# Kernel optimization log

Hardware: AMD Instinct MI355X
Metric: run time of the kernel (lower is better)

The kernel has to match this reference:

```python
import jax, jax.numpy as jnp
import numpy as np

N_NODES = 50000
N_EDGES = 800000
D_IN = 64
N_CLASSES = 2


def _glorot(key, shape):
    lim = float(np.sqrt(6.0 / (shape[0] + shape[1])))
    return jax.random.uniform(key, shape, jnp.float32, -lim, lim)


def setup_inputs() -> dict:
    key = jax.random.key(0)
    ks = jax.random.split(key, 12)
    x = jax.random.normal(ks[0], (N_NODES, D_IN), jnp.float32)
    edge_index = jax.random.randint(ks[1], (2, N_EDGES), 0, N_NODES, jnp.int64)
    return {
        "x": x,
        "edge_index": edge_index,
        # SAGEConv1: 64 -> 16 (lin_l on aggregated neighbors, lin_r on root)
        "w1_n": _glorot(ks[2], (D_IN, 16)), "w1_r": _glorot(ks[3], (D_IN, 16)), "b1": jnp.zeros((16,), jnp.float32),
        # SAGEConv2: 16 -> 32
        "w2_n": _glorot(ks[4], (16, 32)), "w2_r": _glorot(ks[5], (16, 32)), "b2": jnp.zeros((32,), jnp.float32),
        # MLP head
        "fw1": _glorot(ks[6], (32, 64)), "fb1": jnp.zeros((64,), jnp.float32),
        "fw2": _glorot(ks[7], (64, 128)), "fb2": jnp.zeros((128,), jnp.float32),
        "fw3": _glorot(ks[8], (128, N_CLASSES)), "fb3": jnp.zeros((N_CLASSES,), jnp.float32),
    }


def _sage_conv(x, src, dst, w_n, w_r, b):
    # mean aggregation of source-node features onto destination nodes
    msg_sum = jax.ops.segment_sum(x[src], dst, num_segments=N_NODES)  # [N, d]
    deg = jax.ops.segment_sum(jnp.ones((src.shape[0],), x.dtype), dst, num_segments=N_NODES)
    agg = msg_sum / jnp.clip(deg, 1.0)[:, None]
    return agg @ w_n + x @ w_r + b


def reference(x, edge_index, w1_n, w1_r, b1, w2_n, w2_r, b2, fw1, fb1, fw2, fb2, fw3, fb3):
    src, dst = edge_index[0], edge_index[1]
    h = jax.nn.relu(_sage_conv(x, src, dst, w1_n, w1_r, b1))
    h = jax.nn.relu(_sage_conv(h, src, dst, w2_n, w2_r, b2))
    h = jax.nn.relu(h @ fw1 + fb1)
    h = jax.nn.relu(h @ fw2 + fb2)  # dropout omitted (eval mode)
    return h @ fw3 + fb3
```

## Files before the change

kernel.cpp:

```cpp
#include <hip/hip_runtime.h>
#include <hip/hip_fp16.h>

#define N_NODES 50000
#define N_EDGES 800000
#define MAXD 64
#define BSHIFT 7
#define BNODES 128
#define NBUCKET 391
#define NSCB 128
#define EPB (N_EDGES / NSCB)
#define RCAP 64
#define LIN1B ((N_NODES + 63) / 64)

typedef _Float16 f16x8 __attribute__((ext_vector_type(8)));
typedef float f32x4 __attribute__((ext_vector_type(4)));

union H8 { uint4 v; unsigned int u[4]; f16x8 h; };

__device__ __forceinline__ f32x4 MM(const H8& a, const H8& b, f32x4 c) {
    return __builtin_amdgcn_mfma_f32_16x16x32_f16(a.h, b.h, c, 0, 0, 0);
}
__device__ __forceinline__ unsigned int pkh(float a, float b) {
    __half2 h = __floats2half2_rn(a, b);
    unsigned int u;
    __builtin_memcpy(&u, &h, 4);
    return u;
}

__global__ __launch_bounds__(256) void k_scat_lin1(
        const int* __restrict__ src, const int* __restrict__ dst,
        unsigned int* __restrict__ staging, int* __restrict__ counts,
        const float* __restrict__ x,
        const float* __restrict__ w1n, const float* __restrict__ w1r,
        const float* __restrict__ b1,
        __half* __restrict__ xw1n, __half* __restrict__ xr1b) {
    __shared__ __align__(16) unsigned char smem[4608];
    const int tid = threadIdx.x;

    if (blockIdx.x < NSCB) {
        int* lh = (int*)smem;
        for (int i = tid; i < NBUCKET; i += 256) lh[i] = 0;
        __syncthreads();
        const int sb = blockIdx.x;
        const int base = sb * EPB;
        for (int i = tid; i < EPB; i += 256) {
            int d = dst[base + i], s = src[base + i];
            int b = d >> BSHIFT;
            int pos = atomicAdd(&lh[b], 1);
            if (pos < RCAP)
                staging[(b * NSCB + sb) * RCAP + pos] =
                    ((unsigned int)(d & (BNODES - 1)) << 16) | (unsigned int)s;
        }
        __syncthreads();
        for (int i = tid; i < NBUCKET; i += 256)
            counts[i * NSCB + sb] = min(lh[i], RCAP);
    } else {
        __half* s_w1t = (__half*)smem;
        for (int i = tid; i < 2048; i += 256) {
            int o = i & 31, k = i >> 5;
            float v = (o < 16) ? w1n[k * 16 + o] : w1r[k * 16 + (o - 16)];
            s_w1t[o * 72 + k] = __float2half(v);
        }
        __syncthreads();
        const int l = tid & 63, li = l & 15, g = l >> 4;
        const int wid = tid >> 6;
        const int node = (blockIdx.x - NSCB) * 64 + wid * 16 + li;
        const int nodec = node < N_NODES ? node : N_NODES - 1;

        H8 B0, B1;
        {
            const float4* xp = (const float4*)(x + nodec * 64 + 8 * g);
            float4 v0 = xp[0], v1 = xp[1];
            B0.u[0] = pkh(v0.x, v0.y); B0.u[1] = pkh(v0.z, v0.w);
            B0.u[2] = pkh(v1.x, v1.y); B0.u[3] = pkh(v1.z, v1.w);
            const float4* xq = (const float4*)(x + nodec * 64 + 32 + 8 * g);
            float4 w0 = xq[0], w1 = xq[1];
            B1.u[0] = pkh(w0.x, w0.y); B1.u[1] = pkh(w0.z, w0.w);
            B1.u[2] = pkh(w1.x, w1.y); B1.u[3] = pkh(w1.z, w1.w);
        }
        H8 A;
        f32x4 c0 = {0.f, 0.f, 0.f, 0.f};
        A.v = *(const uint4*)(s_w1t + li * 72 + 8 * g);
        c0 = MM(A, B0, c0);
        A.v = *(const uint4*)(s_w1t + li * 72 + 32 + 8 * g);
        c0 = MM(A, B1, c0);
        f32x4 c1 = *(const f32x4*)(b1 + 4 * g);
        A.v = *(const uint4*)(s_w1t + (16 + li) * 72 + 8 * g);
        c1 = MM(A, B0, c1);
        A.v = *(const uint4*)(s_w1t + (16 + li) * 72 + 32 + 8 * g);
        c1 = MM(A, B1, c1);

        if (node < N_NODES) {
            uint2 s0, s1;
            s0.x = pkh(c0[0], c0[1]); s0.y = pkh(c0[2], c0[3]);
            s1.x = pkh(c1[0], c1[1]); s1.y = pkh(c1[2], c1[3]);
            *(uint2*)(xw1n + node * 16 + 4 * g) = s0;
            *(uint2*)(xr1b + node * 16 + 4 * g) = s1;
        }
    }
}

__global__ __launch_bounds__(256) void k_build(
        const unsigned int* __restrict__ staging, const int* __restrict__ counts,
        unsigned int* __restrict__ nbrU, int* __restrict__ deg) {
    __shared__ unsigned short ltbl[BNODES * MAXD];
    __shared__ int lcnt[BNODES];
    __shared__ int lc[NSCB];
    const int tid = threadIdx.x, b = blockIdx.x;
    if (tid < BNODES) lcnt[tid] = 0;
    for (int i = tid; i < NSCB; i += 256) lc[i] = counts[b * NSCB + i];
    __syncthreads();
    for (int i = tid; i < NSCB * RCAP; i += 256) {
        int sb = i >> 6, j = i & 63;
        if (j < lc[sb]) {
            unsigned int u = staging[(b * NSCB + sb) * RCAP + j];
            int dl = u >> 16, s = u & 0xFFFF;
            int slot = atomicAdd(&lcnt[dl], 1);
            if (slot < MAXD) ltbl[(dl << 6) + slot] = (unsigned short)s;
        }
    }
    __syncthreads();
    const int nbase = b << BSHIFT;
    for (int i = tid; i < BNODES * 32; i += 256) {
        int nl = i >> 5, j = i & 31;
        int node = nbase + nl;
        if (node < N_NODES && 2 * j < lcnt[nl]) {
            unsigned int lo = ltbl[(nl << 6) + 2 * j];
            unsigned int hi = ltbl[(nl << 6) + 2 * j + 1];
            nbrU[(node << 5) + j] = lo | (hi << 16);
        }
    }
    if (tid < BNODES && nbase + tid < N_NODES) deg[nbase + tid] = lcnt[tid];
}

__global__ __launch_bounds__(256) void k_agg1(
        const __half* __restrict__ xw1n, const __half* __restrict__ xr1b,
        const int* __restrict__ deg, const unsigned short* __restrict__ nbr,
        __half* __restrict__ h1) {
    const int t = blockIdx.x * 256 + threadIdx.x;
    if (t >= N_NODES * 8) return;
    const int node = t >> 3, fp = t & 7;
    int c = deg[node];
    float inv = c > 0 ? 1.f / (float)c : 1.f;
    int cc = c > MAXD ? MAXD : c;
    const unsigned short* np = nbr + (node << 6);
    float2 a0 = {0.f, 0.f}, a1 = {0.f, 0.f}, a2 = {0.f, 0.f}, a3 = {0.f, 0.f};
    int j = 0;
    for (; j + 4 <= cc; j += 4) {
        float2 v0 = __half22float2(*(const __half2*)(xw1n + (np[j + 0] << 4) + (fp << 1)));
        float2 v1 = __half22float2(*(const __half2*)(xw1n + (np[j + 1] << 4) + (fp << 1)));
        float2 v2 = __half22float2(*(const __half2*)(xw1n + (np[j + 2] << 4) + (fp << 1)));
        float2 v3 = __half22float2(*(const __half2*)(xw1n + (np[j + 3] << 4) + (fp << 1)));
        a0.x += v0.x; a0.y += v0.y; a1.x += v1.x; a1.y += v1.y;
        a2.x += v2.x; a2.y += v2.y; a3.x += v3.x; a3.y += v3.y;
    }
    for (; j < cc; ++j) {
        float2 v = __half22float2(*(const __half2*)(xw1n + (np[j] << 4) + (fp << 1)));
        a0.x += v.x; a0.y += v.y;
    }
    float2 r = __half22float2(*(const __half2*)(xr1b + (node << 4) + (fp << 1)));
    float rx = fmaxf((a0.x + a1.x + a2.x + a3.x) * inv + r.x, 0.f);
    float ry = fmaxf((a0.y + a1.y + a2.y + a3.y) * inv + r.y, 0.f);
    *(__half2*)(h1 + (node << 4) + (fp << 1)) = __floats2half2_rn(rx, ry);
}

__global__ __launch_bounds__(256) void k_head(
        const __half* __restrict__ h1,
        const int* __restrict__ deg, const unsigned short* __restrict__ nbr,
        const float* __restrict__ w2n, const float* __restrict__ w2r,
        const float* __restrict__ b2,
        const float* __restrict__ fw1, const float* __restrict__ fb1,
        const float* __restrict__ fw2, const float* __restrict__ fb2,
        const float* __restrict__ fw3, const float* __restrict__ fb3,
        float* __restrict__ out) {
    __shared__ __align__(16) __half s_w2t[32 * 40];
    __shared__ __align__(16) __half s_fw1t[64 * 40];
    __shared__ __align__(16) __half s_fw2t[128 * 72];

    const int tid = threadIdx.x;
    for (int i = tid; i < 1024; i += 256) {
        int o = i & 31, k = i >> 5;
        float v = (k < 16) ? w2n[k * 32 + o] : w2r[(k - 16) * 32 + o];
        s_w2t[o * 40 + k] = __float2half(v);
    }
    for (int i = tid; i < 2048; i += 256) {
        int o = i & 63, k = i >> 6;
        s_fw1t[o * 40 + k] = __float2half(fw1[k * 64 + o]);
    }
    for (int i = tid; i < 8192; i += 256) {
        int o = i & 127, k = i >> 7;
        s_fw2t[o * 72 + k] = __float2half(fw2[k * 128 + o]);
    }
    __syncthreads();

    const int l = tid & 63, li = l & 15, g = l >> 4;
    const int wid = tid >> 6;
    const int nbase = blockIdx.x * 64 + wid * 16;
    const int node = nbase + li;
    const int nodec = node < N_NODES ? node : N_NODES - 1;
    const int sl0 = li + 32 * (g & 1), sl1 = sl0 + 16;
    const int tsel = g >> 1;

    unsigned int ua0, ua1;
    {
        const int gnode = nbase + (l >> 2);
        const int gn = gnode < N_NODES ? gnode : N_NODES - 1;
        int c = deg[gn];
        float inv = c > 0 ? 1.f / (float)c : 1.f;
        int cc = c > MAXD ? MAXD : c;
        const unsigned short* np = nbr + (gn << 6);
        const int fo = (l & 3) << 2;
        float ax = 0.f, ay = 0.f, az = 0.f, aw = 0.f;
        int j = 0;
        for (; j + 2 <= cc; j += 2) {
            const __half2* h0 = (const __half2*)(h1 + (np[j] << 4) + fo);
            const __half2* h1p = (const __half2*)(h1 + (np[j + 1] << 4) + fo);
            float2 v0 = __half22float2(h0[0]), v1 = __half22float2(h0[1]);
            float2 w0 = __half22float2(h1p[0]), w1 = __half22float2(h1p[1]);
            ax += v0.x + w0.x; ay += v0.y + w0.y;
            az += v1.x + w1.x; aw += v1.y + w1.y;
        }
        if (j < cc) {
            const __half2* h0 = (const __half2*)(h1 + (np[j] << 4) + fo);
            float2 v0 = __half22float2(h0[0]), v1 = __half22float2(h0[1]);
            ax += v0.x; ay += v0.y; az += v1.x; aw += v1.y;
        }
        ua0 = pkh(ax * inv, ay * inv);
        ua1 = pkh(az * inv, aw * inv);
    }
    H8 Bz;
    {
        const int sl = (li << 2) + ((g & 1) << 1);
        Bz.u[0] = (unsigned int)__shfl((int)ua0, sl);
        Bz.u[1] = (unsigned int)__shfl((int)ua1, sl);
        Bz.u[2] = (unsigned int)__shfl((int)ua0, sl + 1);
        Bz.u[3] = (unsigned int)__shfl((int)ua1, sl + 1);
        if (g >= 2)
            Bz.v = *(const uint4*)(h1 + (nodec << 4) + ((g & 1) << 3));
    }

    unsigned int p01[2], p23[2];
#pragma unroll
    for (int t = 0; t < 2; ++t) {
        f32x4 c = *(const f32x4*)(b2 + 16 * t + 4 * g);
        H8 A; A.v = *(const uint4*)(s_w2t + (16 * t + li) * 40 + 8 * g);
        c = MM(A, Bz, c);
        p01[t] = pkh(fmaxf(c[0], 0.f), fmaxf(c[1], 0.f));
        p23[t] = pkh(fmaxf(c[2], 0.f), fmaxf(c[3], 0.f));
    }
    H8 Bh2;
    {
        unsigned int a, b;
        a = __shfl((int)p01[0], sl0); b = __shfl((int)p01[1], sl0); Bh2.u[0] = tsel ? b : a;
        a = __shfl((int)p23[0], sl0); b = __shfl((int)p23[1], sl0); Bh2.u[1] = tsel ? b : a;
        a = __shfl((int)p01[0], sl1); b = __shfl((int)p01[1], sl1); Bh2.u[2] = tsel ? b : a;
        a = __shfl((int)p23[0], sl1); b = __shfl((int)p23[1], sl1); Bh2.u[3] = tsel ? b : a;
    }

    unsigned int q01[4], q23[4];
#pragma unroll
    for (int t = 0; t < 4; ++t) {
        f32x4 c = *(const f32x4*)(fb1 + 16 * t + 4 * g);
        H8 A; A.v = *(const uint4*)(s_fw1t + (16 * t + li) * 40 + 8 * g);
        c = MM(A, Bh2, c);
        q01[t] = pkh(fmaxf(c[0], 0.f), fmaxf(c[1], 0.f));
        q23[t] = pkh(fmaxf(c[2], 0.f), fmaxf(c[3], 0.f));
    }
    H8 Bh3[2];
#pragma unroll
    for (int s = 0; s < 2; ++s) {
        unsigned int a, b;
        a = __shfl((int)q01[2 * s], sl0); b = __shfl((int)q01[2 * s + 1], sl0); Bh3[s].u[0] = tsel ? b : a;
        a = __shfl((int)q23[2 * s], sl0); b = __shfl((int)q23[2 * s + 1], sl0); Bh3[s].u[1] = tsel ? b : a;
        a = __shfl((int)q01[2 * s], sl1); b = __shfl((int)q01[2 * s + 1], sl1); Bh3[s].u[2] = tsel ? b : a;
        a = __shfl((int)q23[2 * s], sl1); b = __shfl((int)q23[2 * s + 1], sl1); Bh3[s].u[3] = tsel ? b : a;
    }

    float o0 = 0.f, o1 = 0.f;
#pragma unroll
    for (int m = 0; m < 8; ++m) {
        f32x4 c = *(const f32x4*)(fb2 + 16 * m + 4 * g);
        H8 A;
        A.v = *(const uint4*)(s_fw2t + (16 * m + li) * 72 + 8 * g);
        c = MM(A, Bh3[0], c);
        A.v = *(const uint4*)(s_fw2t + (16 * m + li) * 72 + 32 + 8 * g);
        c = MM(A, Bh3[1], c);
        const float4* wp = (const float4*)(fw3 + (16 * m + 4 * g) * 2);
        float4 wA = wp[0], wB = wp[1];
        float r0 = fmaxf(c[0], 0.f), r1 = fmaxf(c[1], 0.f);
        float r2 = fmaxf(c[2], 0.f), r3 = fmaxf(c[3], 0.f);
        o0 += r0 * wA.x + r1 * wA.z + r2 * wB.x + r3 * wB.z;
        o1 += r0 * wA.y + r1 * wA.w + r2 * wB.y + r3 * wB.w;
    }
    o0 += __shfl_xor(o0, 16); o0 += __shfl_xor(o0, 32);
    o1 += __shfl_xor(o1, 16); o1 += __shfl_xor(o1, 32);
    if (g == 0 && node < N_NODES) {
        float2 r; r.x = o0 + fb3[0]; r.y = o1 + fb3[1];
        *(float2*)(out + node * 2) = r;
    }
}

extern "C" void kernel_launch(void* const* d_in, const int* in_sizes, int n_in,
                              void* d_out, int out_size, void* d_ws, size_t ws_size,
                              hipStream_t stream) {
    const float* x   = (const float*)d_in[0];
    const int*   ei  = (const int*)d_in[1];
    const int*   src = ei;
    const int*   dst = ei + N_EDGES;
    const float* w1n = (const float*)d_in[2];
    const float* w1r = (const float*)d_in[3];
    const float* b1  = (const float*)d_in[4];
    const float* w2n = (const float*)d_in[5];
    const float* w2r = (const float*)d_in[6];
    const float* b2  = (const float*)d_in[7];
    const float* fw1 = (const float*)d_in[8];
    const float* fb1 = (const float*)d_in[9];
    const float* fw2 = (const float*)d_in[10];
    const float* fb2 = (const float*)d_in[11];
    const float* fw3 = (const float*)d_in[12];
    const float* fb3 = (const float*)d_in[13];
    float* out = (float*)d_out;

    unsigned int* staging = (unsigned int*)d_ws;
    int*          counts  = (int*)(staging + NBUCKET * NSCB * RCAP);
    unsigned int* nbrU    = (unsigned int*)(counts + NBUCKET * NSCB);
    int*          deg     = (int*)(nbrU + N_NODES * 32);
    __half*       xw1n    = (__half*)(deg + N_NODES);
    __half*       xr1b    = xw1n + N_EDGES;
    __half*       h1      = xr1b + N_EDGES;

    const unsigned short* nbr = (const unsigned short*)nbrU;

    k_scat_lin1<<<NSCB + LIN1B, 256, 0, stream>>>(src, dst, staging, counts,
                                                  x, w1n, w1r, b1, xw1n, xr1b);
    k_build<<<NBUCKET, 256, 0, stream>>>(staging, counts, nbrU, deg);
    k_agg1<<<(N_NODES * 8 + 255) / 256, 256, 0, stream>>>(xw1n, xr1b, deg, nbr, h1);
    k_head<<<(N_NODES + 63) / 64, 256, 0, stream>>>(h1, deg, nbr, w2n, w2r, b2,
                                                    fw1, fb1, fw2, fb2, fw3, fb3, out);
}
```

Measured before the change: 68.47 us.

## Fuse CSR build with layer-1 aggregation and halve bucket size

Merges the neighbor-table build kernel with the first mean-aggregation kernel, so aggregation reads neighbor indices from shared memory rather than re-reading them from global memory, and one launch is removed. Bucket size drops from 128 to 64 nodes, which doubles the number of build blocks and halves the per-source-block staging capacity. Weight transposes into shared memory now pack two halves per 32-bit store. The smaller staging capacity (32 entries per bucket per source block) raises the chance of silently dropping edges on skewed inputs, and each block does less aggregation work in parallel.

```diff
diff --git a/kernel.cpp b/kernel.cpp
--- a/kernel.cpp
+++ b/kernel.cpp
@@ -4,12 +4,12 @@
 #define N_NODES 50000
 #define N_EDGES 800000
 #define MAXD 64
-#define BSHIFT 7
-#define BNODES 128
-#define NBUCKET 391
+#define BSHIFT 6
+#define BNODES 64
+#define NBUCKET 782
 #define NSCB 128
 #define EPB (N_EDGES / NSCB)
-#define RCAP 64
+#define RCAP 32
 #define LIN1B ((N_NODES + 63) / 64)
 
 typedef _Float16 f16x8 __attribute__((ext_vector_type(8)));
@@ -56,10 +56,11 @@
             counts[i * NSCB + sb] = min(lh[i], RCAP);
     } else {
         __half* s_w1t = (__half*)smem;
-        for (int i = tid; i < 2048; i += 256) {
-            int o = i & 31, k = i >> 5;
-            float v = (o < 16) ? w1n[k * 16 + o] : w1r[k * 16 + (o - 16)];
-            s_w1t[o * 72 + k] = __float2half(v);
+        for (int i = tid; i < 1024; i += 256) {
+            int o = i & 31, kp = i >> 5;
+            const float* W = (o < 16) ? (w1n + o) : (w1r + (o - 16));
+            *(unsigned int*)(s_w1t + o * 72 + 2 * kp) =
+                pkh(W[(2 * kp) * 16], W[(2 * kp + 1) * 16]);
         }
         __syncthreads();
         const int l = tid & 63, li = l & 15, g = l >> 4;
@@ -100,9 +101,11 @@
     }
 }
 
-__global__ __launch_bounds__(256) void k_build(
+__global__ __launch_bounds__(256) void k_buildAgg1(
         const unsigned int* __restrict__ staging, const int* __restrict__ counts,
-        unsigned int* __restrict__ nbrU, int* __restrict__ deg) {
+        const __half* __restrict__ xw1n, const __half* __restrict__ xr1b,
+        unsigned int* __restrict__ nbrU, int* __restrict__ deg,
+        __half* __restrict__ h1) {
     __shared__ unsigned short ltbl[BNODES * MAXD];
     __shared__ int lcnt[BNODES];
     __shared__ int lc[NSCB];
@@ -111,7 +114,7 @@
     for (int i = tid; i < NSCB; i += 256) lc[i] = counts[b * NSCB + i];
     __syncthreads();
     for (int i = tid; i < NSCB * RCAP; i += 256) {
-        int sb = i >> 6, j = i & 63;
+        int sb = i >> 5, j = i & 31;
         if (j < lc[sb]) {
             unsigned int u = staging[(b * NSCB + sb) * RCAP + j];
             int dl = u >> 16, s = u & 0xFFFF;
@@ -131,37 +134,33 @@
         }
     }
     if (tid < BNODES && nbase + tid < N_NODES) deg[nbase + tid] = lcnt[tid];
-}
-
-__global__ __launch_bounds__(256) void k_agg1(
-        const __half* __restrict__ xw1n, const __half* __restrict__ xr1b,
-        const int* __restrict__ deg, const unsigned short* __restrict__ nbr,
-        __half* __restrict__ h1) {
-    const int t = blockIdx.x * 256 + threadIdx.x;
-    if (t >= N_NODES * 8) return;
-    const int node = t >> 3, fp = t & 7;
-    int c = deg[node];
-    float inv = c > 0 ? 1.f / (float)c : 1.f;
-    int cc = c > MAXD ? MAXD : c;
-    const unsigned short* np = nbr + (node << 6);
-    float2 a0 = {0.f, 0.f}, a1 = {0.f, 0.f}, a2 = {0.f, 0.f}, a3 = {0.f, 0.f};
-    int j = 0;
-    for (; j + 4 <= cc; j += 4) {
-        float2 v0 = __half22float2(*(const __half2*)(xw1n + (np[j + 0] << 4) + (fp << 1)));
-        float2 v1 = __half22float2(*(const __half2*)(xw1n + (np[j + 1] << 4) + (fp << 1)));
-        float2 v2 = __half22float2(*(const __half2*)(xw1n + (np[j + 2] << 4) + (fp << 1)));
-        float2 v3 = __half22float2(*(const __half2*)(xw1n + (np[j + 3] << 4) + (fp << 1)));
-        a0.x += v0.x; a0.y += v0.y; a1.x += v1.x; a1.y += v1.y;
-        a2.x += v2.x; a2.y += v2.y; a3.x += v3.x; a3.y += v3.y;
-    }
-    for (; j < cc; ++j) {
-        float2 v = __half22float2(*(const __half2*)(xw1n + (np[j] << 4) + (fp << 1)));
-        a0.x += v.x; a0.y += v.y;
-    }
-    float2 r = __half22float2(*(const __half2*)(xr1b + (node << 4) + (fp << 1)));
-    float rx = fmaxf((a0.x + a1.x + a2.x + a3.x) * inv + r.x, 0.f);
-    float ry = fmaxf((a0.y + a1.y + a2.y + a3.y) * inv + r.y, 0.f);
-    *(__half2*)(h1 + (node << 4) + (fp << 1)) = __floats2half2_rn(rx, ry);
+    for (int i = tid; i < BNODES * 8; i += 256) {
+        int nl = i >> 3, fp = i & 7;
+        int node = nbase + nl;
+        if (node >= N_NODES) continue;
+        int c = lcnt[nl];
+        float inv = c > 0 ? 1.f / (float)c : 1.f;
+        int cc = c > MAXD ? MAXD : c;
+        const unsigned short* np = ltbl + (nl << 6);
+        float2 a0 = {0.f, 0.f}, a1 = {0.f, 0.f}, a2 = {0.f, 0.f}, a3 = {0.f, 0.f};
+        int j = 0;
+        for (; j + 4 <= cc; j += 4) {
+            float2 v0 = __half22float2(*(const __half2*)(xw1n + (np[j + 0] << 4) + (fp << 1)));
+            float2 v1 = __half22float2(*(const __half2*)(xw1n + (np[j + 1] << 4) + (fp << 1)));
+            float2 v2 = __half22float2(*(const __half2*)(xw1n + (np[j + 2] << 4) + (fp << 1)));
+            float2 v3 = __half22float2(*(const __half2*)(xw1n + (np[j + 3] << 4) + (fp << 1)));
+            a0.x += v0.x; a0.y += v0.y; a1.x += v1.x; a1.y += v1.y;
+            a2.x += v2.x; a2.y += v2.y; a3.x += v3.x; a3.y += v3.y;
+        }
+        for (; j < cc; ++j) {
+            float2 v = __half22float2(*(const __half2*)(xw1n + (np[j] << 4) + (fp << 1)));
+            a0.x += v.x; a0.y += v.y;
+        }
+        float2 r = __half22float2(*(const __half2*)(xr1b + (node << 4) + (fp << 1)));
+        float rx = fmaxf((a0.x + a1.x + a2.x + a3.x) * inv + r.x, 0.f);
+        float ry = fmaxf((a0.y + a1.y + a2.y + a3.y) * inv + r.y, 0.f);
+        *(__half2*)(h1 + (node << 4) + (fp << 1)) = __floats2half2_rn(rx, ry);
+    }
 }
 
 __global__ __launch_bounds__(256) void k_head(
@@ -178,18 +177,24 @@
     __shared__ __align__(16) __half s_fw2t[128 * 72];
 
     const int tid = threadIdx.x;
+    for (int i = tid; i < 512; i += 256) {
+        int o = i & 31, kp = i >> 5;
+        const float* W = (kp < 8) ? (w2n + o) : (w2r + o - 8 * 2 * 32 + 0);
+        float v0, v1;
+        if (kp < 8) { v0 = w2n[(2 * kp) * 32 + o];      v1 = w2n[(2 * kp + 1) * 32 + o]; }
+        else        { v0 = w2r[(2 * kp - 16) * 32 + o]; v1 = w2r[(2 * kp - 15) * 32 + o]; }
+        (void)W;
+        *(unsigned int*)(s_w2t + o * 40 + 2 * kp) = pkh(v0, v1);
+    }
     for (int i = tid; i < 1024; i += 256) {
-        int o = i & 31, k = i >> 5;
-        float v = (k < 16) ? w2n[k * 32 + o] : w2r[(k - 16) * 32 + o];
-        s_w2t[o * 40 + k] = __float2half(v);
-    }
-    for (int i = tid; i < 2048; i += 256) {
-        int o = i & 63, k = i >> 6;
-        s_fw1t[o * 40 + k] = __float2half(fw1[k * 64 + o]);
-    }
-    for (int i = tid; i < 8192; i += 256) {
-        int o = i & 127, k = i >> 7;
-        s_fw2t[o * 72 + k] = __float2half(fw2[k * 128 + o]);
+        int o = i & 63, kp = i >> 6;
+        *(unsigned int*)(s_fw1t + o * 40 + 2 * kp) =
+            pkh(fw1[(2 * kp) * 64 + o], fw1[(2 * kp + 1) * 64 + o]);
+    }
+    for (int i = tid; i < 4096; i += 256) {
+        int o = i & 127, kp = i >> 7;
+        *(unsigned int*)(s_fw2t + o * 72 + 2 * kp) =
+            pkh(fw2[(2 * kp) * 128 + o], fw2[(2 * kp + 1) * 128 + o]);
     }
     __syncthreads();
 
@@ -333,8 +338,8 @@
 
     k_scat_lin1<<<NSCB + LIN1B, 256, 0, stream>>>(src, dst, staging, counts,
                                                   x, w1n, w1r, b1, xw1n, xr1b);
-    k_build<<<NBUCKET, 256, 0, stream>>>(staging, counts, nbrU, deg);
-    k_agg1<<<(N_NODES * 8 + 255) / 256, 256, 0, stream>>>(xw1n, xr1b, deg, nbr, h1);
+    k_buildAgg1<<<NBUCKET, 256, 0, stream>>>(staging, counts, xw1n, xr1b,
+                                             nbrU, deg, h1);
     k_head<<<(N_NODES + 63) / 64, 256, 0, stream>>>(h1, deg, nbr, w2n, w2r, b2,
                                                     fw1, fb1, fw2, fb2, fw3, fb3, out);
 }
```

Result: faster. 63.84 us (-6.8%).
